# Optimization experiments

Measured on AMD Instinct MI355X. Metric: run time of the kernel, lower is better.

The kernel has to match this reference:

```python
import jax, jax.numpy as jnp
import numpy as np


def _conv(x, w, b):
    # NCHW conv with 'same' padding derived from kernel size (matches nn.Conv2d padding=k//2)
    ph, pw = w.shape[2] // 2, w.shape[3] // 2
    y = jax.lax.conv_general_dilated(
        x, w, window_strides=(1, 1), padding=[(ph, ph), (pw, pw)],
        dimension_numbers=("NCHW", "OIHW", "NCHW"))
    return y + b[None, :, None, None]


def _attn(q, k, v):
    # q,k,v: [N,C,H,W]; spatial self-attention over S=H*W positions
    N, C, H, W = q.shape
    S = H * W
    qf = q.reshape(N, C, S)
    kf = k.reshape(N, C, S)
    vf = v.reshape(N, C, S)
    scores = jnp.einsum("ncs,nct->nst", qf, kf) / jnp.sqrt(jnp.asarray(C, qf.dtype))
    a = jax.nn.softmax(scores, axis=-1)
    z = jnp.einsum("nst,nct->ncs", a, vf)
    return z.reshape(N, C, H, W)


def setup_inputs() -> dict:
    key = jax.random.key(0)
    ks = jax.random.split(key, 14)
    B, T, Ci, Hd, H, W = 4, 10, 1, 64, 32, 32
    sc = 0.05
    return {
        "x": jax.random.uniform(ks[0], (B, T, Ci, H, W), jnp.float32),
        # SAConvLSTMCell main conv: (Ci+Hd) -> 4*Hd, 3x3
        "w_conv": jax.random.normal(ks[1], (4 * Hd, Ci + Hd, 3, 3), jnp.float32) * sc,
        "b_conv": jax.random.normal(ks[2], (4 * Hd,), jnp.float32) * sc,
        # SA conv_h: Hd -> 3*Hd, 1x1
        "w_h": jax.random.normal(ks[3], (3 * Hd, Hd, 1, 1), jnp.float32) * sc,
        "b_h": jax.random.normal(ks[4], (3 * Hd,), jnp.float32) * sc,
        # SA conv_m: Hd -> 2*Hd, 1x1
        "w_m": jax.random.normal(ks[5], (2 * Hd, Hd, 1, 1), jnp.float32) * sc,
        "b_m": jax.random.normal(ks[6], (2 * Hd,), jnp.float32) * sc,
        # SA conv_z: 2*Hd -> Hd, 1x1
        "w_z": jax.random.normal(ks[7], (Hd, 2 * Hd, 1, 1), jnp.float32) * sc,
        "b_z": jax.random.normal(ks[8], (Hd,), jnp.float32) * sc,
        # SA conv_output: 2*Hd -> 3*Hd, 3x3
        "w_sa": jax.random.normal(ks[9], (3 * Hd, 2 * Hd, 3, 3), jnp.float32) * sc,
        "b_sa": jax.random.normal(ks[10], (3 * Hd,), jnp.float32) * sc,
        # conv_out: Hd -> Ci, 1x1
        "w_co": jax.random.normal(ks[11], (Ci, Hd, 1, 1), jnp.float32) * sc,
        "b_co": jax.random.normal(ks[12], (Ci,), jnp.float32) * sc,
        "future_frames": 10,
    }


def reference(x, w_conv, b_conv, w_h, b_h, w_m, b_m, w_z, b_z,
              w_sa, b_sa, w_co, b_co, future_frames):
    B, T, Ci, H, W = x.shape
    Hd = w_conv.shape[0] // 4

    def cell(xt, h, c, m):
        cc = _conv(jnp.concatenate([xt, h], axis=1), w_conv, b_conv)
        i, f, o, g = jnp.split(cc, 4, axis=1)
        c_new = jax.nn.sigmoid(f) * c + jax.nn.sigmoid(i) * jnp.tanh(g)
        h_cur = jax.nn.sigmoid(o) * jnp.tanh(c_new)
        # spatial self-attention memory update
        hq, hk, hv = jnp.split(_conv(h_cur, w_h, b_h), 3, axis=1)
        mk, mv = jnp.split(_conv(m, w_m, b_m), 2, axis=1)
        Zh = _attn(hq, hk, hv)
        Zm = _attn(hq, mk, mv)
        Z = _conv(jnp.concatenate([Zh, Zm], axis=1), w_z, b_z)
        i2, g2, o2 = jnp.split(_conv(jnp.concatenate([Z, h_cur], axis=1), w_sa, b_sa), 3, axis=1)
        i2 = jax.nn.sigmoid(i2)
        m_new = i2 * jnp.tanh(g2) + (1.0 - i2) * m
        h_new = jax.nn.sigmoid(o2) * m_new
        return h_new, c_new, m_new

    z = jnp.zeros((B, Hd, H, W), x.dtype)
    state0 = (z, z, z)

    def enc_step(carry, xt):
        h, c, m = carry
        return cell(xt, h, c, m), None

    (h, c, m), _ = jax.lax.scan(enc_step, state0, jnp.moveaxis(x, 1, 0))

    # first decoder input: raw conv_out(h) (no sigmoid, per the original code path)
    inp0 = _conv(h, w_co, b_co)

    def dec_step(carry, _):
        h, c, m, inp = carry
        h, c, m = cell(inp, h, c, m)
        pred = jax.nn.sigmoid(_conv(h, w_co, b_co))
        return (h, c, m, pred), pred

    _, preds = jax.lax.scan(dec_step, (h, c, m, inp0), None, length=future_frames)
    return jnp.moveaxis(preds, 0, 1)  # [B, future_frames, Ci, H, W]
```

## Files before the change

kernel.cpp:

```cpp
#include <hip/hip_runtime.h>
#include <math.h>

#define SS 1024

typedef unsigned short u16;
typedef __attribute__((ext_vector_type(8))) __bf16 bf16x8;
typedef __attribute__((ext_vector_type(4))) float f32x4;

#define MFMA(a,b,c) __builtin_amdgcn_mfma_f32_16x16x32_bf16(a,b,c,0,0,0)

__device__ __forceinline__ float sigm(float x){ return 1.f/(1.f+__expf(-x)); }
__device__ __forceinline__ u16 f2b(float x){ return __builtin_bit_cast(u16,(__bf16)x); }
__device__ __forceinline__ float b2f(u16 u){ return (float)__builtin_bit_cast(__bf16,u); }
__device__ __forceinline__ bf16x8 ldb8(const u16* p){ return *(const bf16x8*)p; }
__device__ __forceinline__ void st4b(u16* p, const f32x4 v){
  union { u16 u[4]; uint2 w; } t;
  t.u[0]=f2b(v[0]); t.u[1]=f2b(v[1]); t.u[2]=f2b(v[2]); t.u[3]=f2b(v[3]);
  *(uint2*)p = t.w;
}

__global__ __launch_bounds__(256) void k_prep(
    const float* __restrict__ wconv, const float* __restrict__ wh,
    const float* __restrict__ wm, const float* __restrict__ wz,
    const float* __restrict__ wsa,
    u16* __restrict__ Wg, u16* __restrict__ Whm,
    u16* __restrict__ Wzp, u16* __restrict__ Wsap)
{
  const int idx = blockIdx.x*256 + threadIdx.x;
  if (idx < 155648) {
    const int step = idx >> 13, co = (idx >> 5) & 255, j = idx & 31;
    float v = 0.f;
    if (step < 18) {
      const int tap = step >> 1, ci = 1 + (step & 1)*32 + j;
      v = wconv[co*585 + ci*9 + tap];
    } else if (j < 9) {
      v = wconv[co*585 + j];
    }
    Wg[idx] = f2b(v);
    return;
  }
  int l = idx - 155648;
  if (l < 20480) {
    const int step = l / 10240, row = (l >> 5) % 320, j = l & 31;
    const int ci = step*32 + j;
    const float v = (row < 192) ? wh[row*64+ci]*(row < 64 ? 0.125f : 1.f)
                                : wm[(row-192)*64+ci];
    Whm[l] = f2b(v);
    return;
  }
  l -= 20480;
  if (l < 8192) {
    const int step = l >> 11, co = (l >> 5) & 63, j = l & 31;
    Wzp[l] = f2b(wz[co*128 + step*32 + j]);
    return;
  }
  l -= 8192;
  if (l < 221184) {
    const int step = l / 6144, co = (l >> 5) % 192, j = l & 31;
    const int tap = step >> 2, ci = (step & 3)*32 + j;
    Wsap[l] = f2b(wsa[(co*128+ci)*9 + tap]);
  }
}

__global__ __launch_bounds__(256) void k_A(
    const u16* __restrict__ hTb, const float* __restrict__ xsrc, int xbs,
    const u16* __restrict__ Wg, const float* __restrict__ bconv,
    float* __restrict__ cT, u16* __restrict__ xcat,
    const u16* __restrict__ mTb, const u16* __restrict__ Whm,
    const float* __restrict__ bh, const float* __restrict__ bm,
    u16* __restrict__ qT, u16* __restrict__ kT, u16* __restrict__ mkT,
    u16* __restrict__ vC, u16* __restrict__ mvC)
{
  __shared__ u16 hcl[16][72];
  const int b = blockIdx.y, s0 = blockIdx.x*16;
  const int tid = threadIdx.x, wid = tid>>6, lane = tid&63, gl = lane>>4, n = lane&15;
  const u16* hb = hTb + (size_t)b*SS*64;
  const int s = s0 + n, y = s>>5, x = s&31;
  f32x4 acc[4];
#pragma unroll
  for (int g4 = 0; g4 < 4; ++g4) {
    const int co = g4*64 + wid*16 + gl*4;
    acc[g4] = (f32x4){ bconv[co], bconv[co+1], bconv[co+2], bconv[co+3] };
  }
  bf16x8 xb;
  {
    union { u16 u[8]; bf16x8 v; } t;
#pragma unroll
    for (int j = 0; j < 8; ++j) t.u[j] = 0;
    if (gl == 0) {
#pragma unroll
      for (int j = 0; j < 8; ++j) {
        const int dy = j/3 - 1, dx = j%3 - 1;
        if ((unsigned)(y+dy) < 32u && (unsigned)(x+dx) < 32u)
          t.u[j] = f2b(xsrc[b*xbs + s + dy*32 + dx]);
      }
    } else if (gl == 1) {
      if (y+1 < 32 && x+1 < 32) t.u[0] = f2b(xsrc[b*xbs + s + 33]);
    }
    xb = t.v;
  }
#pragma unroll
  for (int step = 0; step < 18; ++step) {
    const int tap = step>>1, half = step&1;
    const int dy = tap/3 - 1, dx = tap%3 - 1;
    const bool ok = ((unsigned)(y+dy) < 32u) & ((unsigned)(x+dx) < 32u);
    const int sc = ok ? (s + dy*32 + dx) : s;
    bf16x8 bv = ldb8(hb + (size_t)sc*64 + half*32 + gl*8);
    bv = ok ? bv : (bf16x8){};
#pragma unroll
    for (int g4 = 0; g4 < 4; ++g4) {
      const bf16x8 a = ldb8(Wg + step*8192 + (g4*64 + wid*16 + n)*32 + gl*8);
      acc[g4] = MFMA(a, bv, acc[g4]);
    }
  }
#pragma unroll
  for (int g4 = 0; g4 < 4; ++g4) {
    const bf16x8 a = ldb8(Wg + 18*8192 + (g4*64 + wid*16 + n)*32 + gl*8);
    acc[g4] = MFMA(a, xb, acc[g4]);
  }
  const int hd0 = wid*16 + gl*4;
  {
    float* cp = cT + ((size_t)b*SS + s)*64 + hd0;
    f32x4 cv = *(f32x4*)cp, hcv;
#pragma unroll
    for (int rr = 0; rr < 4; ++rr) {
      const float cn = sigm(acc[1][rr])*cv[rr] + sigm(acc[0][rr])*tanhf(acc[3][rr]);
      cv[rr] = cn;
      hcv[rr] = sigm(acc[2][rr])*tanhf(cn);
    }
    *(f32x4*)cp = cv;
    st4b(xcat + ((size_t)b*SS + s)*128 + 64 + hd0, hcv);
    st4b(&hcl[n][hd0], hcv);
  }
  __syncthreads();
  const int r0 = wid*16, cb = r0 + gl*4;
  f32x4 a1[5];
  a1[0] = (f32x4){ bh[cb]*0.125f, bh[cb+1]*0.125f, bh[cb+2]*0.125f, bh[cb+3]*0.125f };
  a1[1] = (f32x4){ bh[64+cb], bh[64+cb+1], bh[64+cb+2], bh[64+cb+3] };
  a1[2] = (f32x4){ bh[128+cb], bh[128+cb+1], bh[128+cb+2], bh[128+cb+3] };
  a1[3] = (f32x4){ bm[cb], bm[cb+1], bm[cb+2], bm[cb+3] };
  a1[4] = (f32x4){ bm[64+cb], bm[64+cb+1], bm[64+cb+2], bm[64+cb+3] };
#pragma unroll
  for (int step = 0; step < 2; ++step) {
    const bf16x8 bhc = ldb8(&hcl[n][step*32 + gl*8]);
    const bf16x8 bmm = ldb8(mTb + ((size_t)b*SS+s)*64 + step*32 + gl*8);
#pragma unroll
    for (int tt = 0; tt < 5; ++tt) {
      const bf16x8 a = ldb8(Whm + step*10240 + (tt*64 + r0 + n)*32 + gl*8);
      a1[tt] = MFMA(a, tt < 3 ? bhc : bmm, a1[tt]);
    }
  }
  const size_t ps = ((size_t)b*SS + s)*64 + cb;
  st4b(qT + ps, a1[0]);
  st4b(kT + ps, a1[1]);
  st4b(mkT + ps, a1[3]);
#pragma unroll
  for (int rr = 0; rr < 4; ++rr) {
    vC[((size_t)b*64 + cb + rr)*SS + s] = f2b(a1[2][rr]);
    mvC[((size_t)b*64 + cb + rr)*SS + s] = f2b(a1[4][rr]);
  }
}

__global__ __launch_bounds__(256) void k_B(
    const u16* __restrict__ qT, const u16* __restrict__ kT,
    const u16* __restrict__ mkT, const u16* __restrict__ vC,
    const u16* __restrict__ mvC,
    const u16* __restrict__ Wzp, const float* __restrict__ bz,
    u16* __restrict__ xcat)
{
  __shared__ u16 ldsP[4*16*72];
  __shared__ float oS[2][16][65];
  __shared__ float mS[2][16], lS[2][16];
  __shared__ u16 zbuf[16][136];
  const int tid = threadIdx.x, wid = tid>>6, lane = tid&63, gl = lane>>4, n = lane&15;
  const int b = blockIdx.z ? 0 : blockIdx.y, s0 = blockIdx.x*16;
  const int at = wid & 1, kv = wid >> 1;
  const u16* qb = qT + (size_t)b*SS*64;
  const u16* kb = (at ? mkT : kT) + (size_t)b*SS*64;
  const u16* vb = (at ? mvC : vC) + (size_t)b*64*SS;
  const bf16x8 bq0 = ldb8(qb + (size_t)(s0+n)*64 + gl*8);
  const bf16x8 bq1 = ldb8(qb + (size_t)(s0+n)*64 + 32 + gl*8);
  f32x4 o[4];
#pragma unroll
  for (int ct = 0; ct < 4; ++ct) o[ct] = (f32x4){0.f,0.f,0.f,0.f};
  float mrun = -1e30f, lrun = 0.f;
  u16* pb = ldsP + wid*1152 + n*72;

  for (int step = 0; step < 8; ++step) {
    const int t0 = kv*512 + step*64;
    f32x4 st4[4];
#pragma unroll
    for (int tt = 0; tt < 4; ++tt) {
      const u16* kr = kb + (size_t)(t0 + tt*16 + n)*64;
      f32x4 a = {0.f,0.f,0.f,0.f};
      a = MFMA(ldb8(kr + gl*8), bq0, a);
      a = MFMA(ldb8(kr + 32 + gl*8), bq1, a);
      st4[tt] = a;
    }
    float mt = -1e30f;
#pragma unroll
    for (int tt = 0; tt < 4; ++tt)
#pragma unroll
      for (int rr = 0; rr < 4; ++rr) mt = fmaxf(mt, st4[tt][rr]);
    mt = fmaxf(mt, __shfl_xor(mt, 16));
    mt = fmaxf(mt, __shfl_xor(mt, 32));
    const float mnew = fmaxf(mrun, mt);
    const float f = __expf(mrun - mnew);
    float ps = 0.f;
#pragma unroll
    for (int tt = 0; tt < 4; ++tt) {
      const float p0e = __expf(st4[tt][0]-mnew), p1e = __expf(st4[tt][1]-mnew);
      const float p2e = __expf(st4[tt][2]-mnew), p3e = __expf(st4[tt][3]-mnew);
      ps += (p0e + p1e) + (p2e + p3e);
      *(unsigned*)(pb + tt*16 + gl*4)     = (unsigned)f2b(p0e) | ((unsigned)f2b(p1e)<<16);
      *(unsigned*)(pb + tt*16 + gl*4 + 2) = (unsigned)f2b(p2e) | ((unsigned)f2b(p3e)<<16);
    }
    ps += __shfl_xor(ps, 16);
    ps += __shfl_xor(ps, 32);
    lrun = lrun*f + ps;
    mrun = mnew;
    float fr[4];
#pragma unroll
    for (int rr = 0; rr < 4; ++rr) fr[rr] = __shfl(f, gl*4 + rr);
#pragma unroll
    for (int ct = 0; ct < 4; ++ct)
#pragma unroll
      for (int rr = 0; rr < 4; ++rr) o[ct][rr] *= fr[rr];
    const bf16x8 pa0 = ldb8(pb + gl*8);
    const bf16x8 pa1 = ldb8(pb + 32 + gl*8);
#pragma unroll
    for (int ct = 0; ct < 4; ++ct) {
      const u16* vr = vb + (size_t)(ct*16 + n)*SS + t0;
      o[ct] = MFMA(pa0, ldb8(vr + gl*8), o[ct]);
      o[ct] = MFMA(pa1, ldb8(vr + 32 + gl*8), o[ct]);
    }
  }
  if (kv == 1) {
#pragma unroll
    for (int ct = 0; ct < 4; ++ct)
#pragma unroll
      for (int rr = 0; rr < 4; ++rr) oS[at][gl*4+rr][ct*16+n] = o[ct][rr];
    if (gl == 0) { mS[at][n] = mrun; lS[at][n] = lrun; }
  }
  __syncthreads();
  if (kv == 0) {
    const float m1 = mS[at][n], l1 = lS[at][n];
    const float mm = fmaxf(mrun, m1);
    const float e0 = __expf(mrun - mm), e1 = __expf(m1 - mm);
    const float inv = 1.f / (lrun*e0 + l1*e1);
    const float a0 = e0*inv, a1v = e1*inv;
    float f0r[4], f1r[4];
#pragma unroll
    for (int rr = 0; rr < 4; ++rr) {
      f0r[rr] = __shfl(a0, gl*4 + rr);
      f1r[rr] = __shfl(a1v, gl*4 + rr);
    }
#pragma unroll
    for (int ct = 0; ct < 4; ++ct)
#pragma unroll
      for (int rr = 0; rr < 4; ++rr)
        zbuf[gl*4+rr][at*64 + ct*16 + n] =
            f2b(o[ct][rr]*f0r[rr] + oS[at][gl*4+rr][ct*16+n]*f1r[rr]);
  }
  __syncthreads();
  const int co = wid*16 + gl*4;
  f32x4 acc = (f32x4){ bz[co], bz[co+1], bz[co+2], bz[co+3] };
#pragma unroll
  for (int qq = 0; qq < 4; ++qq) {
    const bf16x8 bv = ldb8(&zbuf[n][qq*32 + gl*8]);
    const bf16x8 a = ldb8(Wzp + qq*2048 + (wid*16 + n)*32 + gl*8);
    acc = MFMA(a, bv, acc);
  }
  st4b(xcat + ((size_t)b*SS + s0 + n)*128 + co, acc);
}

__global__ __launch_bounds__(256) void k_C(
    const u16* __restrict__ xcat, const u16* __restrict__ Wsap,
    const float* __restrict__ bsa,
    float* __restrict__ mT, u16* __restrict__ mTb, u16* __restrict__ hTb,
    const float* __restrict__ wco, const float* __restrict__ bco,
    float* __restrict__ inp, float* __restrict__ out, int mode, int j)
{
  __shared__ float pool[16][17];
  const int b = blockIdx.y, s0 = blockIdx.x*16;
  const int tid = threadIdx.x, wid = tid>>6, lane = tid&63, gl = lane>>4, n = lane&15;
  const int hd0 = wid*16 + gl*4;
  const int s = s0 + n, y = s>>5, x = s&31;
  f32x4 acc[3];
#pragma unroll
  for (int i = 0; i < 3; ++i) {
    const int co = i*64 + hd0;
    acc[i] = (f32x4){ bsa[co], bsa[co+1], bsa[co+2], bsa[co+3] };
  }
#pragma unroll
  for (int step = 0; step < 36; ++step) {
    const int tap = step>>2, qq = step&3;
    const int dy = tap/3 - 1, dx = tap%3 - 1;
    const bool ok = ((unsigned)(y+dy) < 32u) & ((unsigned)(x+dx) < 32u);
    const int sc = ok ? (s + dy*32 + dx) : s;
    bf16x8 bv = ldb8(xcat + ((size_t)b*SS + sc)*128 + qq*32 + gl*8);
    bv = ok ? bv : (bf16x8){};
#pragma unroll
    for (int i = 0; i < 3; ++i) {
      const bf16x8 a = ldb8(Wsap + step*6144 + (i*64 + wid*16 + n)*32 + gl*8);
      acc[i] = MFMA(a, bv, acc[i]);
    }
  }
  float* mp = mT + ((size_t)b*SS + s)*64 + hd0;
  f32x4 mv4 = *(f32x4*)mp, hv;
#pragma unroll
  for (int rr = 0; rr < 4; ++rr) {
    const float i2 = sigm(acc[0][rr]);
    const float mn = i2*tanhf(acc[1][rr]) + (1.f - i2)*mv4[rr];
    mv4[rr] = mn;
    hv[rr] = sigm(acc[2][rr])*mn;
  }
  *(f32x4*)mp = mv4;
  st4b(mTb + ((size_t)b*SS + s)*64 + hd0, mv4);
  st4b(hTb + ((size_t)b*SS + s)*64 + hd0, hv);
  if (mode >= 0) {
    pool[n][wid*4 + gl] = hv[0]*wco[hd0] + hv[1]*wco[hd0+1]
                        + hv[2]*wco[hd0+2] + hv[3]*wco[hd0+3];
    __syncthreads();
    if (tid < 16) {
      float v = bco[0];
#pragma unroll
      for (int i = 0; i < 16; ++i) v += pool[tid][i];
      const int sp = s0 + tid;
      if (mode == 1) {
        v = sigm(v);
        out[((size_t)b*10 + j)*SS + sp] = v;
      }
      inp[b*SS + sp] = v;
    }
  }
}

extern "C" void kernel_launch(void* const* d_in, const int* in_sizes, int n_in,
                              void* d_out, int out_size, void* d_ws, size_t ws_size,
                              hipStream_t stream) {
  const float* x      = (const float*)d_in[0];
  const float* w_conv = (const float*)d_in[1];
  const float* b_conv = (const float*)d_in[2];
  const float* w_h    = (const float*)d_in[3];
  const float* b_h    = (const float*)d_in[4];
  const float* w_m    = (const float*)d_in[5];
  const float* b_m    = (const float*)d_in[6];
  const float* w_z    = (const float*)d_in[7];
  const float* b_z    = (const float*)d_in[8];
  const float* w_sa   = (const float*)d_in[9];
  const float* b_sa   = (const float*)d_in[10];
  const float* w_co   = (const float*)d_in[11];
  const float* b_co   = (const float*)d_in[12];
  float* out = (float*)d_out;

  float* ws  = (float*)d_ws;
  float* cT  = ws;
  float* mT  = ws + 262144;
  float* inp = ws + 524288;
  u16* ub   = (u16*)(ws + 528384);
  u16* hTb  = ub;
  u16* mTb  = ub + 262144;
  u16* xcat = ub + 524288;
  u16* qT   = ub + 1048576;
  u16* kT   = ub + 1310720;
  u16* mkT  = ub + 1572864;
  u16* vC   = ub + 1835008;
  u16* mvC  = ub + 2097152;
  u16* Wg   = ub + 2359296;
  u16* Whm  = ub + 2514944;
  u16* Wzp  = ub + 2535424;
  u16* Wsap = ub + 2543616;

  hipMemsetAsync(ws, 0, (size_t)524288*4, stream);
  hipMemsetAsync(hTb, 0, (size_t)524288*2, stream);
  k_prep<<<dim3(1584), 256, 0, stream>>>(w_conv, w_h, w_m, w_z, w_sa, Wg, Whm, Wzp, Wsap);

  auto cell = [&](const float* xsrc, int xbs, int mode, int j) {
    k_A<<<dim3(64,4), 256, 0, stream>>>(hTb, xsrc, xbs, Wg, b_conv, cT, xcat,
                                        mTb, Whm, b_h, b_m, qT, kT, mkT, vC, mvC);
    k_B<<<dim3(64,4), 256, 0, stream>>>(qT, kT, mkT, vC, mvC, Wzp, b_z, xcat);
    k_C<<<dim3(64,4), 256, 0, stream>>>(xcat, Wsap, b_sa, mT, mTb, hTb,
                                        w_co, b_co, inp, out, mode, j);
  };

  for (int t = 0; t < 10; ++t)
    cell(x + (size_t)t*SS, 10*SS, (t == 9) ? 0 : -1, 0);
  for (int j = 0; j < 10; ++j)
    cell(inp, SS, 1, j);
}
```

Before: 1.072 ms.

## Split reduction dimension across more waves in all three cell kernels

Each of the three per-step kernels now runs more wavefronts per block, 512 or 768 threads instead of 256. k_A splits its 3x3 conv over input channels into two halves and overlaps the m-projection with the gate math. k_B splits the attention key range across four waves per attention and merges their online-softmax states. k_C splits its 36-step conv reduction across three wave groups and sums the partials through shared memory. The aim is to shorten each block's serial MFMA chain and fill the GPU better, since the grid only has 256 blocks, at the cost of extra LDS traffic and synchronisation.

After: 980.8 us. 1.09x faster.

```diff
diff --git a/kernel.cpp b/kernel.cpp
--- a/kernel.cpp
+++ b/kernel.cpp
@@ -62,7 +62,7 @@
   }
 }
 
-__global__ __launch_bounds__(256) void k_A(
+__global__ __launch_bounds__(512) void k_A(
     const u16* __restrict__ hTb, const float* __restrict__ xsrc, int xbs,
     const u16* __restrict__ Wg, const float* __restrict__ bconv,
     float* __restrict__ cT, u16* __restrict__ xcat,
@@ -72,54 +72,73 @@
     u16* __restrict__ vC, u16* __restrict__ mvC)
 {
   __shared__ u16 hcl[16][72];
+  __shared__ float part[4][4][64][4];
   const int b = blockIdx.y, s0 = blockIdx.x*16;
   const int tid = threadIdx.x, wid = tid>>6, lane = tid&63, gl = lane>>4, n = lane&15;
+  const int ww = wid & 3, kh = wid >> 2;
   const u16* hb = hTb + (size_t)b*SS*64;
-  const int s = s0 + n, y = s>>5, x = s&31;
+  const int s = s0 + n, y = s>>5, xx = s&31;
   f32x4 acc[4];
 #pragma unroll
   for (int g4 = 0; g4 < 4; ++g4) {
-    const int co = g4*64 + wid*16 + gl*4;
-    acc[g4] = (f32x4){ bconv[co], bconv[co+1], bconv[co+2], bconv[co+3] };
-  }
-  bf16x8 xb;
-  {
-    union { u16 u[8]; bf16x8 v; } t;
-#pragma unroll
-    for (int j = 0; j < 8; ++j) t.u[j] = 0;
-    if (gl == 0) {
-#pragma unroll
-      for (int j = 0; j < 8; ++j) {
-        const int dy = j/3 - 1, dx = j%3 - 1;
-        if ((unsigned)(y+dy) < 32u && (unsigned)(x+dx) < 32u)
-          t.u[j] = f2b(xsrc[b*xbs + s + dy*32 + dx]);
-      }
-    } else if (gl == 1) {
-      if (y+1 < 32 && x+1 < 32) t.u[0] = f2b(xsrc[b*xbs + s + 33]);
-    }
-    xb = t.v;
-  }
-#pragma unroll
-  for (int step = 0; step < 18; ++step) {
+    if (kh == 0) {
+      const int co = g4*64 + ww*16 + gl*4;
+      acc[g4] = (f32x4){ bconv[co], bconv[co+1], bconv[co+2], bconv[co+3] };
+    } else {
+      acc[g4] = (f32x4){0.f,0.f,0.f,0.f};
+    }
+  }
+#pragma unroll
+  for (int ss = 0; ss < 9; ++ss) {
+    const int step = kh*9 + ss;
     const int tap = step>>1, half = step&1;
     const int dy = tap/3 - 1, dx = tap%3 - 1;
-    const bool ok = ((unsigned)(y+dy) < 32u) & ((unsigned)(x+dx) < 32u);
+    const bool ok = ((unsigned)(y+dy) < 32u) & ((unsigned)(xx+dx) < 32u);
     const int sc = ok ? (s + dy*32 + dx) : s;
     bf16x8 bv = ldb8(hb + (size_t)sc*64 + half*32 + gl*8);
     bv = ok ? bv : (bf16x8){};
 #pragma unroll
     for (int g4 = 0; g4 < 4; ++g4) {
-      const bf16x8 a = ldb8(Wg + step*8192 + (g4*64 + wid*16 + n)*32 + gl*8);
+      const bf16x8 a = ldb8(Wg + step*8192 + (g4*64 + ww*16 + n)*32 + gl*8);
       acc[g4] = MFMA(a, bv, acc[g4]);
     }
   }
-#pragma unroll
-  for (int g4 = 0; g4 < 4; ++g4) {
-    const bf16x8 a = ldb8(Wg + 18*8192 + (g4*64 + wid*16 + n)*32 + gl*8);
-    acc[g4] = MFMA(a, xb, acc[g4]);
-  }
-  const int hd0 = wid*16 + gl*4;
-  {
+  if (kh == 1) {
+    bf16x8 xb;
+    {
+      union { u16 u[8]; bf16x8 v; } t;
+#pragma unroll
+      for (int jj = 0; jj < 8; ++jj) t.u[jj] = 0;
+      if (gl == 0) {
+#pragma unroll
+        for (int jj = 0; jj < 8; ++jj) {
+          const int dy = jj/3 - 1, dx = jj%3 - 1;
+          if ((unsigned)(y+dy) < 32u && (unsigned)(xx+dx) < 32u)
+            t.u[jj] = f2b(xsrc[b*xbs + s + dy*32 + dx]);
+        }
+      } else if (gl == 1) {
+        if (y+1 < 32 && xx+1 < 32) t.u[0] = f2b(xsrc[b*xbs + s + 33]);
+      }
+      xb = t.v;
+    }
+#pragma unroll
+    for (int g4 = 0; g4 < 4; ++g4) {
+      const bf16x8 a = ldb8(Wg + 18*8192 + (g4*64 + ww*16 + n)*32 + gl*8);
+      acc[g4] = MFMA(a, xb, acc[g4]);
+    }
+#pragma unroll
+    for (int g4 = 0; g4 < 4; ++g4)
+      *(f32x4*)&part[ww][g4][lane][0] = acc[g4];
+  }
+  __syncthreads();
+  const int r0 = ww*16, cb = r0 + gl*4;
+  if (kh == 0) {
+#pragma unroll
+    for (int g4 = 0; g4 < 4; ++g4) {
+      const f32x4 p = *(const f32x4*)&part[ww][g4][lane][0];
+      acc[g4][0]+=p[0]; acc[g4][1]+=p[1]; acc[g4][2]+=p[2]; acc[g4][3]+=p[3];
+    }
+    const int hd0 = cb;
     float* cp = cT + ((size_t)b*SS + s)*64 + hd0;
     f32x4 cv = *(f32x4*)cp, hcv;
 #pragma unroll
@@ -131,49 +150,55 @@
     *(f32x4*)cp = cv;
     st4b(xcat + ((size_t)b*SS + s)*128 + 64 + hd0, hcv);
     st4b(&hcl[n][hd0], hcv);
+  } else {
+    f32x4 a3 = (f32x4){ bm[cb], bm[cb+1], bm[cb+2], bm[cb+3] };
+    f32x4 a4 = (f32x4){ bm[64+cb], bm[64+cb+1], bm[64+cb+2], bm[64+cb+3] };
+#pragma unroll
+    for (int step = 0; step < 2; ++step) {
+      const bf16x8 bmm = ldb8(mTb + ((size_t)b*SS+s)*64 + step*32 + gl*8);
+      a3 = MFMA(ldb8(Whm + step*10240 + (3*64 + r0 + n)*32 + gl*8), bmm, a3);
+      a4 = MFMA(ldb8(Whm + step*10240 + (4*64 + r0 + n)*32 + gl*8), bmm, a4);
+    }
+    const size_t ps = ((size_t)b*SS + s)*64 + cb;
+    st4b(mkT + ps, a3);
+#pragma unroll
+    for (int rr = 0; rr < 4; ++rr)
+      mvC[((size_t)b*64 + cb + rr)*SS + s] = f2b(a4[rr]);
   }
   __syncthreads();
-  const int r0 = wid*16, cb = r0 + gl*4;
-  f32x4 a1[5];
-  a1[0] = (f32x4){ bh[cb]*0.125f, bh[cb+1]*0.125f, bh[cb+2]*0.125f, bh[cb+3]*0.125f };
-  a1[1] = (f32x4){ bh[64+cb], bh[64+cb+1], bh[64+cb+2], bh[64+cb+3] };
-  a1[2] = (f32x4){ bh[128+cb], bh[128+cb+1], bh[128+cb+2], bh[128+cb+3] };
-  a1[3] = (f32x4){ bm[cb], bm[cb+1], bm[cb+2], bm[cb+3] };
-  a1[4] = (f32x4){ bm[64+cb], bm[64+cb+1], bm[64+cb+2], bm[64+cb+3] };
-#pragma unroll
-  for (int step = 0; step < 2; ++step) {
-    const bf16x8 bhc = ldb8(&hcl[n][step*32 + gl*8]);
-    const bf16x8 bmm = ldb8(mTb + ((size_t)b*SS+s)*64 + step*32 + gl*8);
-#pragma unroll
-    for (int tt = 0; tt < 5; ++tt) {
-      const bf16x8 a = ldb8(Whm + step*10240 + (tt*64 + r0 + n)*32 + gl*8);
-      a1[tt] = MFMA(a, tt < 3 ? bhc : bmm, a1[tt]);
-    }
-  }
-  const size_t ps = ((size_t)b*SS + s)*64 + cb;
-  st4b(qT + ps, a1[0]);
-  st4b(kT + ps, a1[1]);
-  st4b(mkT + ps, a1[3]);
-#pragma unroll
-  for (int rr = 0; rr < 4; ++rr) {
-    vC[((size_t)b*64 + cb + rr)*SS + s] = f2b(a1[2][rr]);
-    mvC[((size_t)b*64 + cb + rr)*SS + s] = f2b(a1[4][rr]);
-  }
-}
-
-__global__ __launch_bounds__(256) void k_B(
+  if (kh == 0) {
+    f32x4 a0 = (f32x4){ bh[cb]*0.125f, bh[cb+1]*0.125f, bh[cb+2]*0.125f, bh[cb+3]*0.125f };
+    f32x4 a1 = (f32x4){ bh[64+cb], bh[64+cb+1], bh[64+cb+2], bh[64+cb+3] };
+    f32x4 a2 = (f32x4){ bh[128+cb], bh[128+cb+1], bh[128+cb+2], bh[128+cb+3] };
+#pragma unroll
+    for (int step = 0; step < 2; ++step) {
+      const bf16x8 bhc = ldb8(&hcl[n][step*32 + gl*8]);
+      a0 = MFMA(ldb8(Whm + step*10240 + (0*64 + r0 + n)*32 + gl*8), bhc, a0);
+      a1 = MFMA(ldb8(Whm + step*10240 + (1*64 + r0 + n)*32 + gl*8), bhc, a1);
+      a2 = MFMA(ldb8(Whm + step*10240 + (2*64 + r0 + n)*32 + gl*8), bhc, a2);
+    }
+    const size_t ps = ((size_t)b*SS + s)*64 + cb;
+    st4b(qT + ps, a0);
+    st4b(kT + ps, a1);
+#pragma unroll
+    for (int rr = 0; rr < 4; ++rr)
+      vC[((size_t)b*64 + cb + rr)*SS + s] = f2b(a2[rr]);
+  }
+}
+
+__global__ __launch_bounds__(512) void k_B(
     const u16* __restrict__ qT, const u16* __restrict__ kT,
     const u16* __restrict__ mkT, const u16* __restrict__ vC,
     const u16* __restrict__ mvC,
     const u16* __restrict__ Wzp, const float* __restrict__ bz,
     u16* __restrict__ xcat)
 {
-  __shared__ u16 ldsP[4*16*72];
-  __shared__ float oS[2][16][65];
-  __shared__ float mS[2][16], lS[2][16];
+  __shared__ u16 ldsP[8*16*72];
+  __shared__ float oS[2][3][16][65];
+  __shared__ float mS[2][3][16], lS[2][3][16];
   __shared__ u16 zbuf[16][136];
   const int tid = threadIdx.x, wid = tid>>6, lane = tid&63, gl = lane>>4, n = lane&15;
-  const int b = blockIdx.z ? 0 : blockIdx.y, s0 = blockIdx.x*16;
+  const int b = blockIdx.y, s0 = blockIdx.x*16;
   const int at = wid & 1, kv = wid >> 1;
   const u16* qb = qT + (size_t)b*SS*64;
   const u16* kb = (at ? mkT : kT) + (size_t)b*SS*64;
@@ -186,8 +211,9 @@
   float mrun = -1e30f, lrun = 0.f;
   u16* pb = ldsP + wid*1152 + n*72;
 
-  for (int step = 0; step < 8; ++step) {
-    const int t0 = kv*512 + step*64;
+#pragma unroll 1
+  for (int step = 0; step < 4; ++step) {
+    const int t0 = kv*256 + step*64;
     f32x4 st4[4];
 #pragma unroll
     for (int tt = 0; tt < 4; ++tt) {
@@ -235,92 +261,123 @@
       o[ct] = MFMA(pa1, ldb8(vr + 32 + gl*8), o[ct]);
     }
   }
-  if (kv == 1) {
+  if (kv > 0) {
 #pragma unroll
     for (int ct = 0; ct < 4; ++ct)
 #pragma unroll
-      for (int rr = 0; rr < 4; ++rr) oS[at][gl*4+rr][ct*16+n] = o[ct][rr];
-    if (gl == 0) { mS[at][n] = mrun; lS[at][n] = lrun; }
+      for (int rr = 0; rr < 4; ++rr) oS[at][kv-1][gl*4+rr][ct*16+n] = o[ct][rr];
+    if (gl == 0) { mS[at][kv-1][n] = mrun; lS[at][kv-1][n] = lrun; }
   }
   __syncthreads();
   if (kv == 0) {
-    const float m1 = mS[at][n], l1 = lS[at][n];
-    const float mm = fmaxf(mrun, m1);
+    const float m1 = mS[at][0][n], m2 = mS[at][1][n], m3 = mS[at][2][n];
+    const float l1 = lS[at][0][n], l2 = lS[at][1][n], l3 = lS[at][2][n];
+    const float mm = fmaxf(fmaxf(mrun, m1), fmaxf(m2, m3));
     const float e0 = __expf(mrun - mm), e1 = __expf(m1 - mm);
-    const float inv = 1.f / (lrun*e0 + l1*e1);
-    const float a0 = e0*inv, a1v = e1*inv;
-    float f0r[4], f1r[4];
+    const float e2 = __expf(m2 - mm),   e3 = __expf(m3 - mm);
+    const float inv = 1.f / (lrun*e0 + l1*e1 + l2*e2 + l3*e3);
+    const float a0 = e0*inv, a1v = e1*inv, a2v = e2*inv, a3v = e3*inv;
+    float f0r[4], f1r[4], f2r[4], f3r[4];
 #pragma unroll
     for (int rr = 0; rr < 4; ++rr) {
       f0r[rr] = __shfl(a0, gl*4 + rr);
       f1r[rr] = __shfl(a1v, gl*4 + rr);
+      f2r[rr] = __shfl(a2v, gl*4 + rr);
+      f3r[rr] = __shfl(a3v, gl*4 + rr);
     }
 #pragma unroll
     for (int ct = 0; ct < 4; ++ct)
 #pragma unroll
-      for (int rr = 0; rr < 4; ++rr)
-        zbuf[gl*4+rr][at*64 + ct*16 + n] =
-            f2b(o[ct][rr]*f0r[rr] + oS[at][gl*4+rr][ct*16+n]*f1r[rr]);
+      for (int rr = 0; rr < 4; ++rr) {
+        const int q = gl*4 + rr, c = ct*16 + n;
+        zbuf[q][at*64 + c] = f2b(o[ct][rr]*f0r[rr] + oS[at][0][q][c]*f1r[rr]
+                                 + oS[at][1][q][c]*f2r[rr] + oS[at][2][q][c]*f3r[rr]);
+      }
   }
   __syncthreads();
-  const int co = wid*16 + gl*4;
-  f32x4 acc = (f32x4){ bz[co], bz[co+1], bz[co+2], bz[co+3] };
-#pragma unroll
-  for (int qq = 0; qq < 4; ++qq) {
-    const bf16x8 bv = ldb8(&zbuf[n][qq*32 + gl*8]);
-    const bf16x8 a = ldb8(Wzp + qq*2048 + (wid*16 + n)*32 + gl*8);
-    acc = MFMA(a, bv, acc);
-  }
-  st4b(xcat + ((size_t)b*SS + s0 + n)*128 + co, acc);
-}
-
-__global__ __launch_bounds__(256) void k_C(
+  if (wid < 4) {
+    const int co = wid*16 + gl*4;
+    f32x4 acc = (f32x4){ bz[co], bz[co+1], bz[co+2], bz[co+3] };
+#pragma unroll
+    for (int qq = 0; qq < 4; ++qq) {
+      const bf16x8 bv = ldb8(&zbuf[n][qq*32 + gl*8]);
+      const bf16x8 a = ldb8(Wzp + qq*2048 + (wid*16 + n)*32 + gl*8);
+      acc = MFMA(a, bv, acc);
+    }
+    st4b(xcat + ((size_t)b*SS + s0 + n)*128 + co, acc);
+  }
+}
+
+__global__ __launch_bounds__(768) void k_C(
     const u16* __restrict__ xcat, const u16* __restrict__ Wsap,
     const float* __restrict__ bsa,
     float* __restrict__ mT, u16* __restrict__ mTb, u16* __restrict__ hTb,
     const float* __restrict__ wco, const float* __restrict__ bco,
     float* __restrict__ inp, float* __restrict__ out, int mode, int j)
 {
+  __shared__ float part[2][4][3][64][4];
   __shared__ float pool[16][17];
   const int b = blockIdx.y, s0 = blockIdx.x*16;
   const int tid = threadIdx.x, wid = tid>>6, lane = tid&63, gl = lane>>4, n = lane&15;
-  const int hd0 = wid*16 + gl*4;
-  const int s = s0 + n, y = s>>5, x = s&31;
+  const int whd = wid & 3, kq = wid >> 2;
+  const int hd0 = whd*16 + gl*4;
+  const int s = s0 + n, y = s>>5, xx = s&31;
   f32x4 acc[3];
 #pragma unroll
   for (int i = 0; i < 3; ++i) {
-    const int co = i*64 + hd0;
-    acc[i] = (f32x4){ bsa[co], bsa[co+1], bsa[co+2], bsa[co+3] };
-  }
-#pragma unroll
-  for (int step = 0; step < 36; ++step) {
+    if (kq == 0) {
+      const int co = i*64 + hd0;
+      acc[i] = (f32x4){ bsa[co], bsa[co+1], bsa[co+2], bsa[co+3] };
+    } else {
+      acc[i] = (f32x4){0.f,0.f,0.f,0.f};
+    }
+  }
+#pragma unroll
+  for (int ss = 0; ss < 12; ++ss) {
+    const int step = kq*12 + ss;
     const int tap = step>>2, qq = step&3;
     const int dy = tap/3 - 1, dx = tap%3 - 1;
-    const bool ok = ((unsigned)(y+dy) < 32u) & ((unsigned)(x+dx) < 32u);
+    const bool ok = ((unsigned)(y+dy) < 32u) & ((unsigned)(xx+dx) < 32u);
     const int sc = ok ? (s + dy*32 + dx) : s;
     bf16x8 bv = ldb8(xcat + ((size_t)b*SS + sc)*128 + qq*32 + gl*8);
     bv = ok ? bv : (bf16x8){};
 #pragma unroll
     for (int i = 0; i < 3; ++i) {
-      const bf16x8 a = ldb8(Wsap + step*6144 + (i*64 + wid*16 + n)*32 + gl*8);
+      const bf16x8 a = ldb8(Wsap + step*6144 + (i*64 + whd*16 + n)*32 + gl*8);
       acc[i] = MFMA(a, bv, acc[i]);
     }
   }
-  float* mp = mT + ((size_t)b*SS + s)*64 + hd0;
-  f32x4 mv4 = *(f32x4*)mp, hv;
-#pragma unroll
-  for (int rr = 0; rr < 4; ++rr) {
-    const float i2 = sigm(acc[0][rr]);
-    const float mn = i2*tanhf(acc[1][rr]) + (1.f - i2)*mv4[rr];
-    mv4[rr] = mn;
-    hv[rr] = sigm(acc[2][rr])*mn;
-  }
-  *(f32x4*)mp = mv4;
-  st4b(mTb + ((size_t)b*SS + s)*64 + hd0, mv4);
-  st4b(hTb + ((size_t)b*SS + s)*64 + hd0, hv);
+  if (kq > 0) {
+#pragma unroll
+    for (int i = 0; i < 3; ++i)
+      *(f32x4*)&part[kq-1][whd][i][lane][0] = acc[i];
+  }
+  __syncthreads();
+  if (kq == 0) {
+#pragma unroll
+    for (int i = 0; i < 3; ++i) {
+      const f32x4 p0 = *(const f32x4*)&part[0][whd][i][lane][0];
+      const f32x4 p1 = *(const f32x4*)&part[1][whd][i][lane][0];
+      acc[i][0] += p0[0] + p1[0]; acc[i][1] += p0[1] + p1[1];
+      acc[i][2] += p0[2] + p1[2]; acc[i][3] += p0[3] + p1[3];
+    }
+    float* mp = mT + ((size_t)b*SS + s)*64 + hd0;
+    f32x4 mv4 = *(f32x4*)mp, hv;
+#pragma unroll
+    for (int rr = 0; rr < 4; ++rr) {
+      const float i2 = sigm(acc[0][rr]);
+      const float mn = i2*tanhf(acc[1][rr]) + (1.f - i2)*mv4[rr];
+      mv4[rr] = mn;
+      hv[rr] = sigm(acc[2][rr])*mn;
+    }
+    *(f32x4*)mp = mv4;
+    st4b(mTb + ((size_t)b*SS + s)*64 + hd0, mv4);
+    st4b(hTb + ((size_t)b*SS + s)*64 + hd0, hv);
+    if (mode >= 0)
+      pool[n][whd*4 + gl] = hv[0]*wco[hd0] + hv[1]*wco[hd0+1]
+                          + hv[2]*wco[hd0+2] + hv[3]*wco[hd0+3];
+  }
   if (mode >= 0) {
-    pool[n][wid*4 + gl] = hv[0]*wco[hd0] + hv[1]*wco[hd0+1]
-                        + hv[2]*wco[hd0+2] + hv[3]*wco[hd0+3];
     __syncthreads();
     if (tid < 16) {
       float v = bco[0];
@@ -377,10 +434,10 @@
   k_prep<<<dim3(1584), 256, 0, stream>>>(w_conv, w_h, w_m, w_z, w_sa, Wg, Whm, Wzp, Wsap);
 
   auto cell = [&](const float* xsrc, int xbs, int mode, int j) {
-    k_A<<<dim3(64,4), 256, 0, stream>>>(hTb, xsrc, xbs, Wg, b_conv, cT, xcat,
+    k_A<<<dim3(64,4), 512, 0, stream>>>(hTb, xsrc, xbs, Wg, b_conv, cT, xcat,
                                         mTb, Whm, b_h, b_m, qT, kT, mkT, vC, mvC);
-    k_B<<<dim3(64,4), 256, 0, stream>>>(qT, kT, mkT, vC, mvC, Wzp, b_z, xcat);
-    k_C<<<dim3(64,4), 256, 0, stream>>>(xcat, Wsap, b_sa, mT, mTb, hTb,
+    k_B<<<dim3(64,4), 512, 0, stream>>>(qT, kT, mkT, vC, mvC, Wzp, b_z, xcat);
+    k_C<<<dim3(64,4), 768, 0, stream>>>(xcat, Wsap, b_sa, mT, mTb, hTb,
                                         w_co, b_co, inp, out, mode, j);
   };
 
```
